# Kernel optimization log

Hardware: AMD Instinct MI355X
Metric: run time of the kernel (lower is better)

## Reference

```python
import jax, jax.numpy as jnp
import numpy as np

N = 100000
E = 1600000
DIM = 128
HID = 16
HEADS = 4
NUM_CLASSES = 2
NEG_SLOPE = 0.2


def _glorot(key, shape):
    fan_in, fan_out = shape[0], shape[-1]
    lim = jnp.sqrt(6.0 / (fan_in + fan_out))
    return jax.random.uniform(key, shape, jnp.float32, -lim, lim)


def setup_inputs() -> dict:
    key = jax.random.key(0)
    ks = jax.random.split(key, 12)
    x = jax.random.normal(ks[0], (N, DIM), jnp.float32)
    edge_index = jax.random.randint(ks[1], (2, E), 0, N, jnp.int32)
    # conv1: in=DIM, out=HID, heads=HEADS
    W1 = _glorot(ks[2], (DIM, HEADS * HID))
    att_src1 = _glorot(ks[3], (HEADS, HID))
    att_dst1 = _glorot(ks[4], (HEADS, HID))
    b1 = jnp.zeros((HEADS * HID,), jnp.float32)
    # conv2: in=HEADS*HID, out=NUM_CLASSES, heads=1
    W2 = _glorot(ks[5], (HEADS * HID, NUM_CLASSES))
    att_src2 = _glorot(ks[6], (1, NUM_CLASSES))
    att_dst2 = _glorot(ks[7], (1, NUM_CLASSES))
    b2 = jnp.zeros((NUM_CLASSES,), jnp.float32)
    return {"x": x, "edge_index": edge_index, "W1": W1, "att_src1": att_src1,
            "att_dst1": att_dst1, "b1": b1, "W2": W2, "att_src2": att_src2,
            "att_dst2": att_dst2, "b2": b2}


def gat_conv(x, src, dst, W, a_src, a_dst, bias, heads, out_ch):
    n = x.shape[0]
    h = (x @ W).reshape(n, heads, out_ch)                      # [N,H,C]
    alpha_s = jnp.sum(h * a_src[None], axis=-1)                # [N,H]
    alpha_d = jnp.sum(h * a_dst[None], axis=-1)                # [N,H]
    e = alpha_s[src] + alpha_d[dst]                            # [Etot,H]
    e = jnp.where(e > 0, e, NEG_SLOPE * e)                     # leaky_relu
    m = jax.ops.segment_max(e, dst, num_segments=n)            # segment softmax
    e = jnp.exp(e - m[dst])
    s = jax.ops.segment_sum(e, dst, num_segments=n)
    alpha = e / (s[dst] + 1e-16)                               # [Etot,H]
    msg = h[src] * alpha[..., None]                            # [Etot,H,C]
    out = jax.ops.segment_sum(msg, dst, num_segments=n)        # [N,H,C]
    return out.reshape(n, heads * out_ch) + bias


def reference(x, edge_index, W1, att_src1, att_dst1, b1, W2, att_src2, att_dst2, b2):
    n = x.shape[0]
    loops = jnp.arange(n, dtype=edge_index.dtype)
    src = jnp.concatenate([edge_index[0], loops])
    dst = jnp.concatenate([edge_index[1], loops])
    # dropout p=0.6 is identity in eval mode
    h = gat_conv(x, src, dst, W1, att_src1, att_dst1, b1, HEADS, HID)
    h = jax.nn.elu(h)
    out = gat_conv(h, src, dst, W2, att_src2, att_dst2, b2, 1, NUM_CLASSES)
    return out
```

## Files before the change

kernel.cpp:

```cpp
#include <hip/hip_runtime.h>
#include <math.h>


#define NB 256
#define BSH 9
#define SRC_MASK 0x1FFFF
#define KC_CHUNK 4096
#define MAXB 12288

static __device__ __forceinline__ unsigned short f2bf(float f) {
    union { float f; unsigned int u; } v; v.f = f;
    unsigned int r = (v.u + 0x7fffu + ((v.u >> 16) & 1u)) >> 16;
    return (unsigned short)r;
}
static __device__ __forceinline__ float bf2f(unsigned short s) {
    union { unsigned int u; float f; } v; v.u = ((unsigned int)s) << 16;
    return v.f;
}
static __device__ __forceinline__ float lrexp(float raw) {
    return __expf(raw > 0.f ? raw : 0.2f * raw);
}

__global__ __launch_bounds__(256) void k_gemm1(const float* __restrict__ x,
                                               const float* __restrict__ W,
                                               float* __restrict__ h1, int n) {
    __shared__ float xs[64 * 132];
    __shared__ float Ws[128 * 64];
    const int t = threadIdx.x;
    const int row0 = blockIdx.x * 64;
    for (int i = t; i < 2048; i += 256)
        ((float4*)Ws)[i] = ((const float4*)W)[i];
    for (int i = t; i < 2048; i += 256) {
        int r = i >> 5, k4 = i & 31;
        float4 v = make_float4(0.f, 0.f, 0.f, 0.f);
        if (row0 + r < n) v = ((const float4*)x)[(size_t)(row0 + r) * 32 + k4];
        *(float4*)&xs[r * 132 + k4 * 4] = v;
    }
    __syncthreads();
    const int tx = t & 15, ty = t >> 4;
    float acc[4][4] = {};
    for (int k = 0; k < 128; k += 4) {
        float4 av[4], bv[4];
#pragma unroll
        for (int i = 0; i < 4; ++i) av[i] = *(const float4*)&xs[(ty * 4 + i) * 132 + k];
#pragma unroll
        for (int kk = 0; kk < 4; ++kk) bv[kk] = *(const float4*)&Ws[(k + kk) * 64 + tx * 4];
#pragma unroll
        for (int kk = 0; kk < 4; ++kk) {
            float4 b = bv[kk];
#pragma unroll
            for (int i = 0; i < 4; ++i) {
                float a = ((const float*)&av[i])[kk];
                acc[i][0] += a * b.x; acc[i][1] += a * b.y;
                acc[i][2] += a * b.z; acc[i][3] += a * b.w;
            }
        }
    }
#pragma unroll
    for (int i = 0; i < 4; ++i) {
        int r = row0 + ty * 4 + i;
        if (r < n) {
            float4 st = make_float4(acc[i][0], acc[i][1], acc[i][2], acc[i][3]);
            ((float4*)h1)[(size_t)r * 16 + tx] = st;
        }
    }
}

__global__ void k_alpha1(const float* __restrict__ h1,
                         const float* __restrict__ att_s,
                         const float* __restrict__ att_d,
                         float* __restrict__ as1, float* __restrict__ ad1,
                         unsigned short* __restrict__ h1b, int n) {
    int i = blockIdx.x * blockDim.x + threadIdx.x;
    if (i >= n * 4) return;
    int node = i >> 2, h = i & 3;
    const float4* hp = (const float4*)(h1 + (size_t)node * 64 + h * 16);
    const float4* sp = (const float4*)(att_s + h * 16);
    const float4* dp = (const float4*)(att_d + h * 16);
    ushort4* bp = (ushort4*)(h1b + (size_t)node * 64 + h * 16);
    float ss = 0.f, dd = 0.f;
#pragma unroll
    for (int q = 0; q < 4; ++q) {
        float4 hv = hp[q], sv = sp[q], dv = dp[q];
        ss += hv.x * sv.x + hv.y * sv.y + hv.z * sv.z + hv.w * sv.w;
        dd += hv.x * dv.x + hv.y * dv.y + hv.z * dv.z + hv.w * dv.w;
        ushort4 b;
        b.x = f2bf(hv.x); b.y = f2bf(hv.y); b.z = f2bf(hv.z); b.w = f2bf(hv.w);
        bp[q] = b;
    }
    as1[i] = ss; ad1[i] = dd;
}

__global__ __launch_bounds__(256) void kA_hist(const int* __restrict__ dst,
                                               int* __restrict__ bcount, int E) {
    __shared__ int h[NB];
    int t = threadIdx.x;
    h[t] = 0; __syncthreads();
    int base = blockIdx.x * KC_CHUNK;
#pragma unroll
    for (int k = 0; k < 16; ++k) {
        int i = base + k * 256 + t;
        if (i < E) atomicAdd(&h[dst[i] >> BSH], 1);
    }
    __syncthreads();
    if (h[t]) atomicAdd(&bcount[t], h[t]);
}

__global__ __launch_bounds__(256) void kB_scan(const int* __restrict__ bcount,
                                               int* __restrict__ boffs,
                                               int* __restrict__ bcursor,
                                               int* __restrict__ offs, int n, int E) {
    __shared__ int sm[NB];
    int t = threadIdx.x;
    int v = bcount[t];
    sm[t] = v; __syncthreads();
    for (int o = 1; o < NB; o <<= 1) {
        int xv = (t >= o) ? sm[t - o] : 0;
        __syncthreads();
        sm[t] += xv; __syncthreads();
    }
    boffs[t + 1] = sm[t];
    bcursor[t] = sm[t] - v;
    if (t == 0) { boffs[0] = 0; offs[n] = E; }
}

__global__ __launch_bounds__(256) void kC_bin(const int* __restrict__ src,
                                              const int* __restrict__ dst,
                                              int* __restrict__ bcursor,
                                              unsigned int* __restrict__ staged, int E) {
    __shared__ unsigned int pairs[KC_CHUNK];
    __shared__ unsigned char binOf[KC_CHUNK];
    __shared__ int h[NB], lofs[NB], lcur[NB], gbase[NB];
    int t = threadIdx.x;
    int base = blockIdx.x * KC_CHUNK;
    int cnt = E - base; if (cnt > KC_CHUNK) cnt = KC_CHUNK;
    h[t] = 0; __syncthreads();
    unsigned int myV[16]; int myBin[16];
#pragma unroll
    for (int k = 0; k < 16; ++k) {
        int li = k * 256 + t;
        myBin[k] = -1;
        if (li < cnt) {
            int gi = base + li;
            int s = src[gi], d = dst[gi];
            int bin = d >> BSH;
            myV[k] = ((unsigned int)(d & ((1 << BSH) - 1)) << 17) | (unsigned int)s;
            myBin[k] = bin;
            atomicAdd(&h[bin], 1);
        }
    }
    __syncthreads();
    int hv = h[t];
    lofs[t] = hv; __syncthreads();
    for (int o = 1; o < NB; o <<= 1) {
        int xv = (t >= o) ? lofs[t - o] : 0;
        __syncthreads();
        lofs[t] += xv; __syncthreads();
    }
    int excl = lofs[t] - hv;
    if (hv) gbase[t] = atomicAdd(&bcursor[t], hv);
    __syncthreads();
    lofs[t] = excl; lcur[t] = excl;
    __syncthreads();
#pragma unroll
    for (int k = 0; k < 16; ++k) {
        if (myBin[k] >= 0) {
            int p = atomicAdd(&lcur[myBin[k]], 1);
            pairs[p] = myV[k];
            binOf[p] = (unsigned char)myBin[k];
        }
    }
    __syncthreads();
    for (int i = t; i < cnt; i += 256) {
        int b = binOf[i];
        staged[gbase[b] + (i - lofs[b])] = pairs[i];
    }
}

__global__ __launch_bounds__(256) void kD_group(const unsigned int* __restrict__ staged,
                                                const int* __restrict__ boffs,
                                                const float* __restrict__ as1,
                                                const float* __restrict__ ad1,
                                                unsigned int* __restrict__ grouped,
                                                float4* __restrict__ w4,
                                                int* __restrict__ offs, int n) {
    __shared__ int lh[512], lofs2[512], lcur2[512];
    __shared__ unsigned int st[MAXB];
    int t = threadIdx.x;
    int b = blockIdx.x;
    int base = boffs[b];
    int cnt = boffs[b + 1] - base;
    lh[t] = 0; lh[t + 256] = 0;
    __syncthreads();
    for (int i = t; i < cnt; i += 256)
        atomicAdd(&lh[staged[base + i] >> 17], 1);
    __syncthreads();
    int a0 = lh[2 * t], a1 = lh[2 * t + 1];
    int sp = a0 + a1;
    lcur2[t] = sp; __syncthreads();
    for (int o = 1; o < NB; o <<= 1) {
        int xv = (t >= o) ? lcur2[t - o] : 0;
        __syncthreads();
        lcur2[t] += xv; __syncthreads();
    }
    int excl = lcur2[t] - sp;
    lofs2[2 * t] = excl; lofs2[2 * t + 1] = excl + a0;
    __syncthreads();
#pragma unroll
    for (int q = 0; q < 2; ++q) {
        int dl = t + q * 256;
        int d = (b << BSH) + dl;
        if (d < n) offs[d] = base + lofs2[dl];
        lcur2[dl] = lofs2[dl];
    }
    __syncthreads();
    for (int i = t; i < cnt; i += 256) {
        unsigned int v = staged[base + i];
        int p = atomicAdd(&lcur2[v >> 17], 1);
        st[p] = v;
    }
    __syncthreads();
    for (int i = t; i < cnt; i += 256) {
        unsigned int v = st[i];
        int s = (int)(v & SRC_MASK);
        int d = (b << BSH) + (int)(v >> 17);
        float4 a = ((const float4*)as1)[s];
        float4 ad = ((const float4*)ad1)[d];
        float4 w;
        w.x = lrexp(a.x + ad.x); w.y = lrexp(a.y + ad.y);
        w.z = lrexp(a.z + ad.z); w.w = lrexp(a.w + ad.w);
        grouped[base + i] = v;
        w4[base + i] = w;
    }
}

__global__ __launch_bounds__(256) void k_agg1(
        const int* __restrict__ offs, const unsigned int* __restrict__ grouped,
        const float* __restrict__ w4,
        const unsigned short* __restrict__ h1b, const float* __restrict__ as1,
        const float* __restrict__ ad1, const float* __restrict__ b1,
        float* __restrict__ out1, int n) {
    const int lane = threadIdx.x & 63;
    const int d = blockIdx.x * 4 + (threadIdx.x >> 6);
    if (d >= n) return;
    const int c = lane;
    const int h = lane >> 4;
    const int sub = lane & 15;
    const int off0 = offs[d], off1 = offs[d + 1];
    const int total = off1 - off0 + 1;
    const float wselfv = lrexp(as1[d * 4 + h] + ad1[d * 4 + h]);

    float acc = 0.f, wsum = 0.f;
    for (int base = 0; base < total; base += 16) {
        int e = base + sub;
        float w = 0.f; int s = d;
        if (e < total) {
            if (e < total - 1) {
                unsigned int v = grouped[off0 + e];
                s = (int)(v & SRC_MASK);
                w = w4[(size_t)(off0 + e) * 4 + h];
            } else {
                w = wselfv;
            }
        }
        wsum += w;
#pragma unroll
        for (int j = 0; j < 16; ++j) {
            int sj = __builtin_amdgcn_readlane(s, j);
            float wj = __shfl(w, (h << 4) + j);
            acc += wj * bf2f(h1b[(size_t)sj * 64 + c]);
        }
    }
    wsum += __shfl_xor(wsum, 1);
    wsum += __shfl_xor(wsum, 2);
    wsum += __shfl_xor(wsum, 4);
    wsum += __shfl_xor(wsum, 8);
    out1[(size_t)d * 64 + c] = acc / (wsum + 1e-16f) + b1[c];
}

__global__ void k_node2(const float* __restrict__ out1, const float* __restrict__ W2,
                        const float* __restrict__ att_s2, const float* __restrict__ att_d2,
                        float4* __restrict__ pack, int n) {
    int i = blockIdx.x * blockDim.x + threadIdx.x;
    if (i >= n) return;
    const float4* row = (const float4*)(out1 + (size_t)i * 64);
    float h0 = 0.f, h1v = 0.f;
#pragma unroll
    for (int q = 0; q < 16; ++q) {
        float4 v = row[q];
        float e0 = v.x > 0.f ? v.x : expm1f(v.x);
        float e1 = v.y > 0.f ? v.y : expm1f(v.y);
        float e2 = v.z > 0.f ? v.z : expm1f(v.z);
        float e3 = v.w > 0.f ? v.w : expm1f(v.w);
        int k = q * 4;
        h0  += e0 * W2[(k + 0) * 2 + 0] + e1 * W2[(k + 1) * 2 + 0]
             + e2 * W2[(k + 2) * 2 + 0] + e3 * W2[(k + 3) * 2 + 0];
        h1v += e0 * W2[(k + 0) * 2 + 1] + e1 * W2[(k + 1) * 2 + 1]
             + e2 * W2[(k + 2) * 2 + 1] + e3 * W2[(k + 3) * 2 + 1];
    }
    pack[i] = make_float4(h0, h1v,
                          h0 * att_s2[0] + h1v * att_s2[1],
                          h0 * att_d2[0] + h1v * att_d2[1]);
}

__global__ __launch_bounds__(256) void k_agg2(
        const int* __restrict__ offs, const unsigned int* __restrict__ grouped,
        const float4* __restrict__ pack, const float* __restrict__ b2,
        float* __restrict__ out, int n) {
    int t = threadIdx.x;
    int g = blockIdx.x * 16 + (t >> 4);
    int sub = t & 15;
    if (g >= n) return;
    int off0 = offs[g], off1 = offs[g + 1];
    int total = off1 - off0 + 1;
    float ad = pack[g].w;
    float a0 = 0.f, a1 = 0.f, ws = 0.f;
    for (int e = sub; e < total; e += 16) {
        int s = (e == total - 1) ? g : (int)(grouped[off0 + e] & SRC_MASK);
        float4 ps = pack[s];
        float w = lrexp(ps.z + ad);
        a0 += w * ps.x; a1 += w * ps.y; ws += w;
    }
#pragma unroll
    for (int m = 1; m < 16; m <<= 1) {
        a0 += __shfl_xor(a0, m);
        a1 += __shfl_xor(a1, m);
        ws += __shfl_xor(ws, m);
    }
    if (sub == 0) {
        float inv = 1.f / (ws + 1e-16f);
        out[(size_t)g * 2 + 0] = a0 * inv + b2[0];
        out[(size_t)g * 2 + 1] = a1 * inv + b2[1];
    }
}

extern "C" void kernel_launch(void* const* d_in, const int* in_sizes, int n_in,
                              void* d_out, int out_size, void* d_ws, size_t ws_size,
                              hipStream_t stream) {
    const float* x    = (const float*)d_in[0];
    const int*   ei   = (const int*)d_in[1];
    const float* W1   = (const float*)d_in[2];
    const float* as1w = (const float*)d_in[3];
    const float* ad1w = (const float*)d_in[4];
    const float* b1   = (const float*)d_in[5];
    const float* W2   = (const float*)d_in[6];
    const float* as2w = (const float*)d_in[7];
    const float* ad2w = (const float*)d_in[8];
    const float* b2   = (const float*)d_in[9];
    const int n = in_sizes[0] / 128;
    const int E = in_sizes[1] / 2;
    float* out = (float*)d_out;

    char* ws = (char*)d_ws;
    size_t off = 0;
    auto alloc = [&](size_t bytes) {
        void* p = ws + off;
        off = (off + bytes + 255) & ~(size_t)255;
        return p;
    };
    float*  h1     = (float*)alloc((size_t)n * 64 * 4);
    float*  out1   = (float*)alloc((size_t)n * 64 * 4);
    unsigned short* h1b = (unsigned short*)alloc((size_t)n * 64 * 2);
    float*  as1    = (float*)alloc((size_t)n * 4 * 4);
    float*  ad1    = (float*)alloc((size_t)n * 4 * 4);
    float4* pack   = (float4*)alloc((size_t)n * 16);
    int*    offs   = (int*)alloc((size_t)(n + 1) * 4);
    int*    bcount = (int*)alloc(NB * 4);
    int*    boffs  = (int*)alloc((NB + 1) * 4);
    int*    bcursor= (int*)alloc(NB * 4);
    unsigned int* staged  = (unsigned int*)alloc((size_t)E * 4);
    unsigned int* grouped = (unsigned int*)alloc((size_t)E * 4);
    float*  w4     = (float*)alloc((size_t)E * 4 * 4);

    hipMemsetAsync(bcount, 0, NB * 4, stream);

    const int nblk = (E + KC_CHUNK - 1) / KC_CHUNK;
    k_gemm1<<<(n + 63) / 64, 256, 0, stream>>>(x, W1, h1, n);
    k_alpha1<<<(n * 4 + 255) / 256, 256, 0, stream>>>(h1, as1w, ad1w, as1, ad1, h1b, n);
    kA_hist<<<nblk, 256, 0, stream>>>(ei + E, bcount, E);
    kB_scan<<<1, 256, 0, stream>>>(bcount, boffs, bcursor, offs, n, E);
    kC_bin<<<nblk, 256, 0, stream>>>(ei, ei + E, bcursor, staged, E);
    kD_group<<<NB, 256, 0, stream>>>(staged, boffs, as1, ad1, grouped, (float4*)w4, offs, n);
    k_agg1<<<(n + 3) / 4, 256, 0, stream>>>(offs, grouped, w4, h1b, as1, ad1, b1, out1, n);
    k_node2<<<(n + 255) / 256, 256, 0, stream>>>(out1, W2, as2w, ad2w, pack, n);
    k_agg2<<<(n + 15) / 16, 256, 0, stream>>>(offs, grouped, pack, b2, out, n);
}
```

Baseline: 281.1 us.

## Fuse attention logits into GEMM epilogue and compute edge weights on the fly

The attention dot products and the bf16 conversion move into the first GEMM's epilogue, using a shared-memory reduction across the 16 column threads. This removes the fp32 h1 intermediate and the separate alpha kernel. The per-edge exp weight buffer w4 is also dropped: kD_group now only writes grouped indices, and k_agg1 recomputes each weight from as1[src] plus ad1[dst]. That saves 16 bytes per edge of writes and reads, at the cost of an extra scattered as1 gather and an exp per edge inside the aggregation loop.

```diff
diff --git a/kernel.cpp b/kernel.cpp
--- a/kernel.cpp
+++ b/kernel.cpp
@@ -23,7 +23,11 @@
 
 __global__ __launch_bounds__(256) void k_gemm1(const float* __restrict__ x,
                                                const float* __restrict__ W,
-                                               float* __restrict__ h1, int n) {
+                                               const float* __restrict__ att_s,
+                                               const float* __restrict__ att_d,
+                                               unsigned short* __restrict__ h1b,
+                                               float* __restrict__ as1,
+                                               float* __restrict__ ad1, int n) {
     __shared__ float xs[64 * 132];
     __shared__ float Ws[128 * 64];
     const int t = threadIdx.x;
@@ -56,39 +60,41 @@
             }
         }
     }
+    float4 sv = ((const float4*)att_s)[tx];
+    float4 dv = ((const float4*)att_d)[tx];
+    float ps[4], pd[4];
 #pragma unroll
     for (int i = 0; i < 4; ++i) {
+        ps[i] = acc[i][0] * sv.x + acc[i][1] * sv.y + acc[i][2] * sv.z + acc[i][3] * sv.w;
+        pd[i] = acc[i][0] * dv.x + acc[i][1] * dv.y + acc[i][2] * dv.z + acc[i][3] * dv.w;
         int r = row0 + ty * 4 + i;
         if (r < n) {
-            float4 st = make_float4(acc[i][0], acc[i][1], acc[i][2], acc[i][3]);
-            ((float4*)h1)[(size_t)r * 16 + tx] = st;
-        }
-    }
-}
-
-__global__ void k_alpha1(const float* __restrict__ h1,
-                         const float* __restrict__ att_s,
-                         const float* __restrict__ att_d,
-                         float* __restrict__ as1, float* __restrict__ ad1,
-                         unsigned short* __restrict__ h1b, int n) {
-    int i = blockIdx.x * blockDim.x + threadIdx.x;
-    if (i >= n * 4) return;
-    int node = i >> 2, h = i & 3;
-    const float4* hp = (const float4*)(h1 + (size_t)node * 64 + h * 16);
-    const float4* sp = (const float4*)(att_s + h * 16);
-    const float4* dp = (const float4*)(att_d + h * 16);
-    ushort4* bp = (ushort4*)(h1b + (size_t)node * 64 + h * 16);
-    float ss = 0.f, dd = 0.f;
-#pragma unroll
-    for (int q = 0; q < 4; ++q) {
-        float4 hv = hp[q], sv = sp[q], dv = dp[q];
-        ss += hv.x * sv.x + hv.y * sv.y + hv.z * sv.z + hv.w * sv.w;
-        dd += hv.x * dv.x + hv.y * dv.y + hv.z * dv.z + hv.w * dv.w;
-        ushort4 b;
-        b.x = f2bf(hv.x); b.y = f2bf(hv.y); b.z = f2bf(hv.z); b.w = f2bf(hv.w);
-        bp[q] = b;
-    }
-    as1[i] = ss; ad1[i] = dd;
+            ushort4 b;
+            b.x = f2bf(acc[i][0]); b.y = f2bf(acc[i][1]);
+            b.z = f2bf(acc[i][2]); b.w = f2bf(acc[i][3]);
+            ((ushort4*)h1b)[(size_t)r * 16 + tx] = b;
+        }
+    }
+    __syncthreads();
+    float* redA = xs;
+    float* redB = xs + 1024;
+#pragma unroll
+    for (int i = 0; i < 4; ++i) {
+        int row = ty * 4 + i;
+        redA[row * 16 + tx] = ps[i];
+        redB[row * 16 + tx] = pd[i];
+    }
+    __syncthreads();
+    {
+        int row = t >> 2, h = t & 3;
+        int r = row0 + row;
+        if (r < n) {
+            const float* pa = &redA[row * 16 + h * 4];
+            const float* pb = &redB[row * 16 + h * 4];
+            as1[r * 4 + h] = pa[0] + pa[1] + pa[2] + pa[3];
+            ad1[r * 4 + h] = pb[0] + pb[1] + pb[2] + pb[3];
+        }
+    }
 }
 
 __global__ __launch_bounds__(256) void kA_hist(const int* __restrict__ dst,
@@ -179,10 +185,7 @@
 
 __global__ __launch_bounds__(256) void kD_group(const unsigned int* __restrict__ staged,
                                                 const int* __restrict__ boffs,
-                                                const float* __restrict__ as1,
-                                                const float* __restrict__ ad1,
                                                 unsigned int* __restrict__ grouped,
-                                                float4* __restrict__ w4,
                                                 int* __restrict__ offs, int n) {
     __shared__ int lh[512], lofs2[512], lcur2[512];
     __shared__ unsigned int st[MAXB];
@@ -220,23 +223,12 @@
         st[p] = v;
     }
     __syncthreads();
-    for (int i = t; i < cnt; i += 256) {
-        unsigned int v = st[i];
-        int s = (int)(v & SRC_MASK);
-        int d = (b << BSH) + (int)(v >> 17);
-        float4 a = ((const float4*)as1)[s];
-        float4 ad = ((const float4*)ad1)[d];
-        float4 w;
-        w.x = lrexp(a.x + ad.x); w.y = lrexp(a.y + ad.y);
-        w.z = lrexp(a.z + ad.z); w.w = lrexp(a.w + ad.w);
-        grouped[base + i] = v;
-        w4[base + i] = w;
-    }
+    for (int i = t; i < cnt; i += 256)
+        grouped[base + i] = st[i];
 }
 
 __global__ __launch_bounds__(256) void k_agg1(
         const int* __restrict__ offs, const unsigned int* __restrict__ grouped,
-        const float* __restrict__ w4,
         const unsigned short* __restrict__ h1b, const float* __restrict__ as1,
         const float* __restrict__ ad1, const float* __restrict__ b1,
         float* __restrict__ out1, int n) {
@@ -248,7 +240,8 @@
     const int sub = lane & 15;
     const int off0 = offs[d], off1 = offs[d + 1];
     const int total = off1 - off0 + 1;
-    const float wselfv = lrexp(as1[d * 4 + h] + ad1[d * 4 + h]);
+    const float adh = ad1[d * 4 + h];
+    const float wselfv = lrexp(as1[d * 4 + h] + adh);
 
     float acc = 0.f, wsum = 0.f;
     for (int base = 0; base < total; base += 16) {
@@ -258,7 +251,7 @@
             if (e < total - 1) {
                 unsigned int v = grouped[off0 + e];
                 s = (int)(v & SRC_MASK);
-                w = w4[(size_t)(off0 + e) * 4 + h];
+                w = lrexp(as1[s * 4 + h] + adh);
             } else {
                 w = wselfv;
             }
@@ -358,7 +351,6 @@
         off = (off + bytes + 255) & ~(size_t)255;
         return p;
     };
-    float*  h1     = (float*)alloc((size_t)n * 64 * 4);
     float*  out1   = (float*)alloc((size_t)n * 64 * 4);
     unsigned short* h1b = (unsigned short*)alloc((size_t)n * 64 * 2);
     float*  as1    = (float*)alloc((size_t)n * 4 * 4);
@@ -370,18 +362,16 @@
     int*    bcursor= (int*)alloc(NB * 4);
     unsigned int* staged  = (unsigned int*)alloc((size_t)E * 4);
     unsigned int* grouped = (unsigned int*)alloc((size_t)E * 4);
-    float*  w4     = (float*)alloc((size_t)E * 4 * 4);
 
     hipMemsetAsync(bcount, 0, NB * 4, stream);
 
     const int nblk = (E + KC_CHUNK - 1) / KC_CHUNK;
-    k_gemm1<<<(n + 63) / 64, 256, 0, stream>>>(x, W1, h1, n);
-    k_alpha1<<<(n * 4 + 255) / 256, 256, 0, stream>>>(h1, as1w, ad1w, as1, ad1, h1b, n);
+    k_gemm1<<<(n + 63) / 64, 256, 0, stream>>>(x, W1, as1w, ad1w, h1b, as1, ad1, n);
     kA_hist<<<nblk, 256, 0, stream>>>(ei + E, bcount, E);
     kB_scan<<<1, 256, 0, stream>>>(bcount, boffs, bcursor, offs, n, E);
     kC_bin<<<nblk, 256, 0, stream>>>(ei, ei + E, bcursor, staged, E);
-    kD_group<<<NB, 256, 0, stream>>>(staged, boffs, as1, ad1, grouped, (float4*)w4, offs, n);
-    k_agg1<<<(n + 3) / 4, 256, 0, stream>>>(offs, grouped, w4, h1b, as1, ad1, b1, out1, n);
+    kD_group<<<NB, 256, 0, stream>>>(staged, boffs, grouped, offs, n);
+    k_agg1<<<(n + 3) / 4, 256, 0, stream>>>(offs, grouped, h1b, as1, ad1, b1, out1, n);
     k_node2<<<(n + 255) / 256, 256, 0, stream>>>(out1, W2, as2w, ad2w, pack, n);
     k_agg2<<<(n + 15) / 16, 256, 0, stream>>>(offs, grouped, pack, b2, out, n);
 }
```

Result: faster. 260.4 us (-7.4%).
